# Kernel tuning notes

Measured on AMD Instinct MI355X. Metric: run time of the kernel, lower is better.

Reference implementation:

```python
import jax, jax.numpy as jnp
import numpy as np


def conv2d(x, w, b, pad):
    # NCHW conv, stride 1, symmetric padding
    out = jax.lax.conv_general_dilated(
        x, w, window_strides=(1, 1), padding=[(pad, pad), (pad, pad)],
        dimension_numbers=("NCHW", "OIHW", "NCHW"))
    return out + b[None, :, None, None]


def setup_inputs() -> dict:
    key = jax.random.key(0)
    ks = jax.random.split(key, 18)
    B, C, H, W = 4, 256, 64, 64
    Cq = C // 16  # 16
    Ck = C // 8   # 32
    s = 0.02
    return {
        "x": jax.random.normal(ks[0], (B, C, H, W), jnp.float32),
        "dw1_w": jax.random.normal(ks[1], (Cq, C, 7, 7), jnp.float32) * s,
        "dw1_b": jnp.zeros((Cq,), jnp.float32),
        "dw2_w": jax.random.normal(ks[2], (Cq, C, 11, 11), jnp.float32) * s,
        "dw2_b": jnp.zeros((Cq,), jnp.float32),
        "key_w": jax.random.normal(ks[3], (Ck, C, 1, 1), jnp.float32) * s,
        "key_b": jnp.zeros((Ck,), jnp.float32),
        "value_w": jax.random.normal(ks[4], (C, C, 1, 1), jnp.float32) * s,
        "value_b": jnp.zeros((C,), jnp.float32),
        "conv1_w": jax.random.normal(ks[5], (Cq, C, 3, 3), jnp.float32) * s,
        "conv1_b": jnp.zeros((Cq,), jnp.float32),
        "conv2_w": jax.random.normal(ks[6], (C, Cq, 3, 3), jnp.float32) * s,
        "conv2_b": jnp.zeros((C,), jnp.float32),
        "se_w": jax.random.normal(ks[7], (C, C, 1, 1), jnp.float32) * s,
        "se_b": jnp.zeros((C,), jnp.float32),
        "gamma1": jnp.zeros((1,), jnp.float32) + 0.1,  # nonzero so attention path is exercised
        "gamma2": jnp.zeros((1,), jnp.float32) + 0.1,
    }


def reference(x, dw1_w, dw1_b, dw2_w, dw2_b, key_w, key_b, value_w, value_b,
              conv1_w, conv1_b, conv2_w, conv2_b, se_w, se_b, gamma1, gamma2):
    B, C, H, W = x.shape
    HW = H * W
    # q: concat of 7x7 and 11x11 conv branches -> (B, HW, C//8)
    q = jnp.concatenate([conv2d(x, dw1_w, dw1_b, 3), conv2d(x, dw2_w, dw2_b, 5)], axis=1)
    q = q.reshape(B, -1, HW).transpose(0, 2, 1)
    # k: 1x1 conv -> (B, C//8, HW)
    k = conv2d(x, key_w, key_b, 0).reshape(B, -1, HW)
    # raw (unscaled) full spatial attention, softmax over last dim
    att = jax.nn.softmax(jnp.einsum("bnc,bcm->bnm", q, k), axis=-1)  # (B, HW, HW)
    v = conv2d(x, value_w, value_b, 0).reshape(B, C, HW)
    out = jnp.einsum("bcm,bnm->bcn", v, att).reshape(B, C, H, W)
    # local conv branch + channel attention (SE)
    y = conv2d(jax.nn.silu(conv2d(x, conv1_w, conv1_b, 1)), conv2_w, conv2_b, 1)
    pooled = jnp.mean(y, axis=(2, 3), keepdims=True)  # (B, C, 1, 1)
    se = y * jax.nn.sigmoid(conv2d(pooled, se_w, se_b, 0))
    return gamma1 * out + gamma2 * se + x
```

## Files before the change

kernel.cpp:

```cpp
#include <hip/hip_runtime.h>

typedef unsigned short u16;
typedef unsigned u32;
typedef __bf16 bf16x8 __attribute__((ext_vector_type(8)));
typedef float f32x4 __attribute__((ext_vector_type(4)));
typedef float f32x16 __attribute__((ext_vector_type(16)));

#define MFMA16(A,B,C) __builtin_amdgcn_mfma_f32_16x16x32_bf16((A),(B),(C),0,0,0)
#define MFMA32(A,B,C) __builtin_amdgcn_mfma_f32_32x32x16_bf16((A),(B),(C),0,0,0)

__device__ __forceinline__ u16 f2b(float f){
  union { float f; unsigned u; } X; X.f = f;
  unsigned r = X.u + 0x7FFFu + ((X.u >> 16) & 1u);
  return (u16)(r >> 16);
}
__device__ __forceinline__ float b2f(u16 h){
  union { unsigned u; float f; } X; X.u = ((unsigned)h) << 16; return X.f;
}
__device__ __forceinline__ u16 f2b_trunc(float f){
  union { float f; unsigned u; } X; X.f = f;
  return (u16)(X.u >> 16);
}
__device__ __forceinline__ bf16x8 ld_frag(const u16* p){
  union { uint4 u; bf16x8 v; } U; U.u = *(const uint4*)p; return U.v;
}
__device__ __forceinline__ u32 pkbf(float a, float b){
  u32 r; asm("v_cvt_pk_bf16_f32 %0, %1, %2" : "=v"(r) : "v"(a), "v"(b)); return r;
}
__device__ __forceinline__ void pl32swap(u32& x, u32& y){
  auto r = __builtin_amdgcn_permlane32_swap(x, y, false, false);
  x = r[0]; y = r[1];
}
__device__ __forceinline__ void gld16(const u16* g, u16* l){
  __builtin_amdgcn_global_load_lds(
      (const __attribute__((address_space(1))) u32*)g,
      (__attribute__((address_space(3))) u32*)l, 16, 0, 0);
}

__global__ __launch_bounds__(256) void k_prep_w(
    const float* __restrict__ dw1, const float* __restrict__ dw2,
    const float* __restrict__ cw1, const float* __restrict__ kw,
    const float* __restrict__ vw,  const float* __restrict__ cw2,
    u16* __restrict__ wB, u16* __restrict__ wC,
    u16* __restrict__ kwt, u16* __restrict__ vwt, u16* __restrict__ w2t){
  int i = blockIdx.x * 256 + threadIdx.x;
  const int NB = 991232, NC = 73728, NK = 8192, NV = 65536, N2 = 40960;
  if(i < NB){
    int tap = i >> 13, rem = i & 8191;
    int chunk = rem >> 9, r2 = rem & 511;
    int oc = r2 >> 4, ci = chunk*16 + (r2 & 15);
    int dy = tap / 11, dx = tap - dy*11;
    float v;
    if(oc < 16){
      v = (dy >= 2 && dy <= 8 && dx >= 2 && dx <= 8) ? dw1[(oc*256 + ci)*49 + (dy-2)*7 + (dx-2)] : 0.f;
    } else {
      v = dw2[((oc-16)*256 + ci)*121 + tap];
    }
    wB[i] = f2b(v);
    return;
  }
  i -= NB;
  if(i < NC){
    int tap = i >> 13, rem = i & 8191;
    int chunk = rem >> 9, r2 = rem & 511;
    int oc = r2 >> 4, ci = chunk*16 + (r2 & 15);
    wC[i] = (oc < 16) ? f2b(cw1[(oc*256 + ci)*9 + tap]) : (u16)0;
    return;
  }
  i -= NC;
  if(i < NK){ kwt[i] = f2b(kw[i]); return; }
  i -= NK;
  if(i < NV){ vwt[i] = f2b(vw[i]); return; }
  i -= NV;
  if(i < N2){
    int co = i/160, kk = i - co*160;
    int tap = kk >> 4, ci = kk & 15;
    w2t[i] = (tap < 9) ? f2b(cw2[co*144 + ci*9 + tap]) : (u16)0;
    return;
  }
}

__global__ __launch_bounds__(256) void k_prep_x(const float* __restrict__ x, u16* __restrict__ xp){
  __shared__ float tile[32][33];
  const int bid = blockIdx.x;
  const int b = bid >> 10, rem = bid & 1023;
  const int c0 = (rem >> 7) << 5, m0 = (rem & 127) << 5;
  const int t = threadIdx.x;
  { const int cg = t >> 5, mm = t & 31;
    #pragma unroll
    for(int i=0;i<4;i++)
      tile[cg*4+i][mm] = x[((size_t)(b*256 + c0 + cg*4 + i) << 12) + m0 + mm];
  }
  __syncthreads();
  { const int cp = (t & 15) << 1, mloc = t >> 4;
    #pragma unroll
    for(int half = 0; half < 2; ++half){
      const int ml = half*16 + mloc;
      const int m = m0 + ml;
      const int yy = (m >> 6) + 5, xx = (m & 63) + 5;
      const int ci = c0 + cp;
      const int chunk = ci >> 4, wi = ci & 15;
      u16 lo = f2b(tile[cp][ml]), hi = f2b(tile[cp+1][ml]);
      *(unsigned*)&xp[(((size_t)(b*16 + chunk)*74 + yy)*80 + xx)*16 + wi] = ((unsigned)hi << 16) | lo;
    }
  }
}

__global__ __launch_bounds__(256) void k_qconv(
    const u16* __restrict__ xp, const u16* __restrict__ wB, const u16* __restrict__ wC,
    u16* __restrict__ qp){
  __shared__ __align__(16) u16 buf[15360];
  const int bid = blockIdx.x;
  const int rg = bid & 31, b = (bid >> 5) & 3, kq = bid >> 7;
  const int y0 = rg << 1;
  const int t = threadIdx.x, wv = t >> 6, lane = t & 63;
  const int m = lane & 31, kh = lane >> 5;
  const int laneoff = m*16 + kh*8;
  const int r = wv & 1, xo = (wv >> 1) << 5;
  const f32x16 z16 = {0.f,0.f,0.f,0.f,0.f,0.f,0.f,0.f,0.f,0.f,0.f,0.f,0.f,0.f,0.f,0.f};
  f32x16 acc = z16, acc1 = z16;

  #pragma unroll 1
  for(int c = 0; c < 2; ++c){
    const int chunk = kq*2 + c;
    const uint4* src = (const uint4*)(xp + ((size_t)((b*16 + chunk)*74 + y0))*1280);
    __syncthreads();
    for(int e = t; e < 1920; e += 256){
      ((uint4*)buf)[(e & 1)*960 + (e >> 1)] = src[e];
    }
    __syncthreads();
    const u16* wBc = wB + chunk*512 + laneoff;
    const u16* wCc = wC + chunk*512 + laneoff;
    const u16* ap = buf + kh*7680 + (r*80 + xo + m)*8;
    #pragma unroll 1
    for(int dy = 0; dy < 11; ++dy){
      const u16* rowp = ap + dy*640;
      const u16* wrow = wBc + dy*11*8192;
      const bool in1y = (dy >= 4) & (dy <= 6);
      #pragma unroll
      for(int dx = 0; dx < 11; ++dx){
        bf16x8 A = ld_frag(rowp + dx*8);
        bf16x8 B = ld_frag(wrow + dx*8192);
        acc = MFMA32(A, B, acc);
        if(in1y && dx >= 4 && dx <= 6){
          bf16x8 B1 = ld_frag(wCc + ((dy-4)*3 + (dx-4))*8192);
          acc1 = MFMA32(A, B1, acc1);
        }
      }
    }
  }

  u16* qb = qp + ((size_t)kq*16384 + (b << 12) + (y0 + r)*64 + xo) * 48;
  #pragma unroll
  for(int reg = 0; reg < 16; ++reg){
    const int row = (reg & 3) + ((reg >> 2) << 3) + (kh << 2);
    qb[row*48 + m] = f2b(acc[reg]);
    if(m < 16) qb[row*48 + 32 + m] = f2b(acc1[reg]);
  }
}

__global__ __launch_bounds__(256) void k_qfin(
    const u16* __restrict__ qp, const float* __restrict__ b7,
    const float* __restrict__ b11, const float* __restrict__ b1,
    u16* __restrict__ q_t, u16* __restrict__ t1){
  const int t = threadIdx.x, wv = t >> 6, lane = t & 63;
  const int px = blockIdx.x*4 + wv;
  if(lane >= 48) return;
  const size_t off = (size_t)px*48 + lane;
  float s = 0.f;
  #pragma unroll
  for(int sp = 0; sp < 8; ++sp) s += b2f(qp[off + (size_t)sp*786432]);
  const float LOG2E = 1.44269504f;
  if(lane < 16){
    q_t[px*32 + lane] = f2b((s + b7[lane]) * LOG2E);
  } else if(lane < 32){
    q_t[px*32 + lane] = f2b((s + b11[lane - 16]) * LOG2E);
  } else {
    float v = s + b1[lane - 32];
    t1[px*16 + lane - 32] = f2b(v / (1.f + __expf(-v)));
  }
}

__global__ __launch_bounds__(256) void k_kv(
    const u16* __restrict__ xp, const u16* __restrict__ vwt, const u16* __restrict__ kwt,
    const float* __restrict__ vb, const float* __restrict__ kb,
    u16* __restrict__ vt, u16* __restrict__ k_t){
  const int bid = blockIdx.x;
  const int h = bid & 3, blk = (bid >> 2) & 63, b = bid >> 8;
  const int wv = threadIdx.x >> 6, lane = threadIdx.x & 63;
  const int col = lane & 15, quad = lane >> 4;
  const int m0 = (blk << 6) + (wv << 4);
  f32x4 z = {0.f,0.f,0.f,0.f};
  f32x4 av[4], ak[2];
  #pragma unroll
  for(int i=0;i<4;i++) av[i] = z;
  ak[0] = z; ak[1] = z;
  const int m = m0 + col;
  const int py = (m >> 6) + 5, pxx = (m & 63) + 5;
  #pragma unroll 1
  for(int ch = 0; ch < 8; ++ch){
    const int cio = ch*32 + quad*8;
    const int chunk = cio >> 4, wi = cio & 15;
    bf16x8 xf = ld_frag(xp + (((size_t)(b*16 + chunk)*74 + py)*80 + pxx)*16 + wi);
    #pragma unroll
    for(int ct2 = 0; ct2 < 4; ++ct2){
      bf16x8 wf = ld_frag(vwt + (((h*4 + ct2)*16 + col) << 8) + cio);
      av[ct2] = MFMA16(wf, xf, av[ct2]);
    }
    if(h == 0){
      #pragma unroll
      for(int kt = 0; kt < 2; ++kt){
        bf16x8 kf = ld_frag(kwt + ((kt*16 + col) << 8) + cio);
        ak[kt] = MFMA16(xf, kf, ak[kt]);
      }
    }
  }
  const int g = m0 >> 5, lo = (m0 & 31) + col;
  #pragma unroll
  for(int ct2 = 0; ct2 < 4; ++ct2){
    #pragma unroll
    for(int r = 0; r < 4; ++r){
      const int c = (h*4 + ct2)*16 + quad*4 + r;
      vt[((size_t)(b*128 + g)*256 + c)*32 + lo] = f2b(av[ct2][r] + vb[c]);
    }
  }
  if(h == 0){
    #pragma unroll
    for(int kt = 0; kt < 2; ++kt){
      #pragma unroll
      for(int r = 0; r < 4; ++r){
        const int mq = b*4096 + m0 + quad*4 + r;
        k_t[mq*32 + kt*16 + col] = f2b((ak[kt][r] + kb[kt*16 + col]) );
      }
    }
  }
}

__global__ __launch_bounds__(512, 4) void k_attn(
    const u16* __restrict__ q_t, const u16* __restrict__ k_t,
    const u16* __restrict__ vt, u16* __restrict__ Op,
    float* __restrict__ lsav){
  __shared__ __align__(16) u16 V[2][16384];
  const int bid = blockIdx.x;
  const int q0 = (bid & 31) << 7, b = (bid >> 5) & 3, ks = bid >> 7;
  const int t = threadIdx.x, wv = t >> 6, lane = t & 63;
  const int cq = lane & 31, hi = lane >> 5;
  const int wq = wv >> 1, ch = wv & 1;
  const int swz = (cq & 7) << 4;
  const int cbase = (ch*128 + cq) * 128;

  const u16* qrow = q_t + ((size_t)(b*4096 + q0 + wq*32 + cq) << 5) + hi*8;
  const bf16x8 qf0 = ld_frag(qrow), qf1 = ld_frag(qrow + 16);
  const u16* kbase = k_t + ((size_t)(b*4096 + ks*1024 + cq) << 5) + hi*8;
  const u16* vsrc = vt + ((size_t)(b*128 + ks*32) << 13);

  u32 srcoff[4];
  #pragma unroll
  for(int s = 0; s < 4; ++s){
    const int idx = s*512 + t;
    const int c = idx >> 3;
    const int rs = ((idx & 7) << 4) ^ ((c & 7) << 4);
    srcoff[s] = ((rs >> 6) << 13) + (c << 5) + ((rs & 63) >> 1);
  }

  const f32x16 z16 = {0.f,0.f,0.f,0.f,0.f,0.f,0.f,0.f,0.f,0.f,0.f,0.f,0.f,0.f,0.f,0.f};
  f32x16 acc0 = z16, acc1 = z16, acc2 = z16, acc3 = z16;
  float lsum = 0.f;

  #pragma unroll
  for(int s = 0; s < 4; ++s)
    gld16(vsrc + srcoff[s], &V[0][s*4096 + (wv << 9)]);
  __syncthreads();

  #pragma unroll 1
  for(int it = 0; it < 16; ++it){
    const int cur = it & 1;
    if(it < 15){
      const u16* gb = vsrc + ((size_t)(it + 1) << 14);
      #pragma unroll
      for(int s = 0; s < 4; ++s)
        gld16(gb + srcoff[s], &V[cur ^ 1][s*4096 + (wv << 9)]);
    }
    const u16* kp = kbase + ((size_t)it << 11);
    const u16* Vb = &V[cur][0];
    #pragma unroll
    for(int sub = 0; sub < 2; ++sub){
      const bf16x8 kf0 = ld_frag(kp + sub*1024);
      const bf16x8 kf1 = ld_frag(kp + sub*1024 + 16);
      f32x16 S = MFMA32(kf0, qf0, z16);
      S = MFMA32(kf1, qf1, S);
      #pragma unroll
      for(int rr = 0; rr < 16; ++rr){ S[rr] = exp2f(S[rr]); lsum += S[rr]; }
      u32 a0 = pkbf(S[0], S[1]),   b0 = pkbf(S[4], S[5]);
      u32 a1 = pkbf(S[2], S[3]),   b1 = pkbf(S[6], S[7]);
      u32 c0 = pkbf(S[8], S[9]),   d0 = pkbf(S[12], S[13]);
      u32 c1 = pkbf(S[10], S[11]), d1 = pkbf(S[14], S[15]);
      pl32swap(a0, b0); pl32swap(a1, b1); pl32swap(c0, d0); pl32swap(c1, d1);
      union { u32 w[4]; bf16x8 v; } A0, A1;
      A0.w[0] = a0; A0.w[1] = a1; A0.w[2] = b0; A0.w[3] = b1;
      A1.w[0] = c0; A1.w[1] = c1; A1.w[2] = d0; A1.w[3] = d1;
      const int o0 = cbase + ((((sub << 6) | (hi << 4))) ^ swz);
      const char* vb0 = (const char*)Vb + o0;
      const char* vb1 = (const char*)Vb + (o0 ^ 32);
      acc0 = MFMA32(A0.v, ld_frag((const u16*)(vb0)),         acc0);
      acc1 = MFMA32(A0.v, ld_frag((const u16*)(vb0 + 4096)),  acc1);
      acc2 = MFMA32(A0.v, ld_frag((const u16*)(vb0 + 8192)),  acc2);
      acc3 = MFMA32(A0.v, ld_frag((const u16*)(vb0 + 12288)), acc3);
      acc0 = MFMA32(A1.v, ld_frag((const u16*)(vb1)),         acc0);
      acc1 = MFMA32(A1.v, ld_frag((const u16*)(vb1 + 4096)),  acc1);
      acc2 = MFMA32(A1.v, ld_frag((const u16*)(vb1 + 8192)),  acc2);
      acc3 = MFMA32(A1.v, ld_frag((const u16*)(vb1 + 12288)), acc3);
    }
    __syncthreads();
  }

  lsum += __shfl_xor(lsum, 32);
  const float invl = 1.f / lsum;
  if(ch == 0 && hi == 0)
    lsav[ks*16384 + b*4096 + q0 + wq*32 + cq] = lsum;
  u16* ob = Op + (((size_t)(ks*16384 + b*4096 + q0 + wq*32)) << 8) + ch*128 + cq;
  #pragma unroll
  for(int reg = 0; reg < 16; ++reg){
    const int row = (reg & 3) + ((reg >> 2) << 3) + (hi << 2);
    const float inv = __shfl(invl, row);
    u16* orow = ob + ((size_t)row << 8);
    orow[0]  = f2b(acc0[reg] * inv);
    orow[32] = f2b(acc1[reg] * inv);
    orow[64] = f2b(acc2[reg] * inv);
    orow[96] = f2b(acc3[reg] * inv);
  }
}

__global__ __launch_bounds__(256) void k_conv2(
    const u16* __restrict__ t1, const u16* __restrict__ w2t, const float* __restrict__ b2,
    u16* __restrict__ y_t, float* __restrict__ pooled){
  __shared__ __align__(16) u16 im[64][168];
  __shared__ float pool_l[64];
  const int bid = blockIdx.x;
  const int h = bid & 3, y = (bid >> 2) & 63, b = bid >> 8;
  const int t = threadIdx.x;
  if(t < 64) pool_l[t] = 0.f;
  const u16* t1b = t1 + ((size_t)(b*4096) << 4);
  { const int px = t >> 2, ci0 = (t & 3) << 2;
    #pragma unroll
    for(int tap = 0; tap < 9; ++tap){
      const int ky = (tap*11) >> 5, kx = tap - ky*3;
      const int ryy = y + ky - 1, rxx = px + kx - 1;
      uint2 val = make_uint2(0u, 0u);
      if((unsigned)ryy < 64u && (unsigned)rxx < 64u)
        val = *(const uint2*)(t1b + (((ryy << 6) + rxx) << 4) + ci0);
      *(uint2*)&im[px][tap*16 + ci0] = val;
    }
    for(int e = t; e < 1024; e += 256){ im[e >> 4][144 + (e & 15)] = 0; }
  }
  __syncthreads();
  const int wv = t >> 6, lane = t & 63, col = lane & 15, quad = lane >> 4;
  const f32x4 z = {0.f,0.f,0.f,0.f};
  f32x4 acc[4];
  #pragma unroll
  for(int i=0;i<4;i++) acc[i] = z;
  #pragma unroll
  for(int ch = 0; ch < 5; ++ch){
    bf16x8 af = ld_frag(&im[wv*16 + col][ch*32 + quad*8]);
    #pragma unroll
    for(int j = 0; j < 4; ++j){
      bf16x8 wf = ld_frag(w2t + ((h*4 + j)*16 + col)*160 + ch*32 + quad*8);
      acc[j] = MFMA16(af, wf, acc[j]);
    }
  }
  const int m0 = (y << 6) + (wv << 4) + (quad << 2);
  #pragma unroll
  for(int j = 0; j < 4; ++j){
    const int c = (h*4 + j)*16 + col;
    const float bias = b2[c];
    float s = 0.f;
    #pragma unroll
    for(int r = 0; r < 4; ++r){
      float v = acc[j][r] + bias;
      y_t[((size_t)(b*4096 + m0 + r) << 8) + c] = f2b(v);
      s += v;
    }
    s += __shfl_xor(s, 16); s += __shfl_xor(s, 32);
    if(quad == 0) atomicAdd(&pool_l[c - h*64], s);
  }
  __syncthreads();
  if(t < 64) atomicAdd(&pooled[b*256 + h*64 + t], pool_l[t]);
}

__global__ __launch_bounds__(256) void k_final(
    const u16* __restrict__ Op, const u16* __restrict__ y_t, const float* __restrict__ x,
    const float* __restrict__ lsav, const float* __restrict__ pooled,
    const float* __restrict__ sew, const float* __restrict__ seb,
    const float* __restrict__ g1p, const float* __restrict__ g2p,
    float* __restrict__ out){
  __shared__ float tO[32][65];
  __shared__ float tY[32][65];
  __shared__ float gate_l[32];
  const int bid = blockIdx.x;
  const int b = bid >> 9, rem = bid & 511;
  const int c0 = (rem >> 6) << 5, m0 = (rem & 63) << 6;
  const int t = threadIdx.x;
  const float g1 = g1p[0], g2 = g2p[0];
  { const int cl = t >> 3, k0 = (t & 7) << 5;
    const int c = c0 + cl;
    const float* wr = sew + (size_t)c*256 + k0;
    const float* pr = pooled + b*256 + k0;
    float part = 0.f;
    #pragma unroll
    for(int j = 0; j < 32; j += 4){
      float4 w4 = *(const float4*)(wr + j);
      float4 p4 = *(const float4*)(pr + j);
      part += w4.x*p4.x + w4.y*p4.y + w4.z*p4.z + w4.w*p4.w;
    }
    part += __shfl_xor(part, 1); part += __shfl_xor(part, 2); part += __shfl_xor(part, 4);
    if((t & 7) == 0){
      float a = part * (1.f/4096.f) + seb[c];
      gate_l[cl] = g2 / (1.f + __expf(-a));
    }
  }
  { const int ml = t >> 2, cg = (t & 3) << 3;
    const int gq = b*4096 + m0 + ml;
    const float l0 = lsav[gq], l1 = lsav[16384 + gq], l2 = lsav[32768 + gq], l3 = lsav[49152 + gq];
    const float inv = 1.f / (l0 + l1 + l2 + l3);
    const float w0 = l0*inv, w1 = l1*inv, w2 = l2*inv, w3 = l3*inv;
    const size_t base = ((size_t)gq << 8) + c0 + cg;
    union { uint4 u; u16 s[8]; } A0, A1, A2, A3;
    A0.u = *(const uint4*)(Op + base);
    A1.u = *(const uint4*)(Op + base + ((size_t)16384 << 8));
    A2.u = *(const uint4*)(Op + base + ((size_t)32768 << 8));
    A3.u = *(const uint4*)(Op + base + ((size_t)49152 << 8));
    #pragma unroll
    for(int i = 0; i < 8; ++i)
      tO[cg+i][ml] = w0*b2f(A0.s[i]) + w1*b2f(A1.s[i]) + w2*b2f(A2.s[i]) + w3*b2f(A3.s[i]);
    const u16* yrow = y_t + base;
    uint4 yu = *(const uint4*)yrow;
    tY[cg+0][ml]=b2f((u16)(yu.x & 0xffffu)); tY[cg+1][ml]=b2f((u16)(yu.x >> 16));
    tY[cg+2][ml]=b2f((u16)(yu.y & 0xffffu)); tY[cg+3][ml]=b2f((u16)(yu.y >> 16));
    tY[cg+4][ml]=b2f((u16)(yu.z & 0xffffu)); tY[cg+5][ml]=b2f((u16)(yu.z >> 16));
    tY[cg+6][ml]=b2f((u16)(yu.w & 0xffffu)); tY[cg+7][ml]=b2f((u16)(yu.w >> 16));
  }
  __syncthreads();
  { const int cl = t >> 3, mg = (t & 7) << 3;
    const int c = c0 + cl;
    const float gate = gate_l[cl];
    const float* xrow = x + ((size_t)(b*256 + c) << 12) + m0 + mg;
    float* orow = out + ((size_t)(b*256 + c) << 12) + m0 + mg;
    float4 x0 = *(const float4*)xrow, x1 = *(const float4*)(xrow + 4);
    float4 r0, r1;
    r0.x = g1*tO[cl][mg+0] + gate*tY[cl][mg+0] + x0.x;
    r0.y = g1*tO[cl][mg+1] + gate*tY[cl][mg+1] + x0.y;
    r0.z = g1*tO[cl][mg+2] + gate*tY[cl][mg+2] + x0.z;
    r0.w = g1*tO[cl][mg+3] + gate*tY[cl][mg+3] + x0.w;
    r1.x = g1*tO[cl][mg+4] + gate*tY[cl][mg+4] + x1.x;
    r1.y = g1*tO[cl][mg+5] + gate*tY[cl][mg+5] + x1.y;
    r1.z = g1*tO[cl][mg+6] + gate*tY[cl][mg+6] + x1.z;
    r1.w = g1*tO[cl][mg+7] + gate*tY[cl][mg+7] + x1.w;
    *(float4*)orow = r0;
    *(float4*)(orow + 4) = r1;
  }
}

extern "C" void kernel_launch(void* const* d_in, const int* in_sizes, int n_in,
                              void* d_out, int out_size, void* d_ws, size_t ws_size,
                              hipStream_t stream){
  (void)in_sizes; (void)n_in; (void)out_size; (void)ws_size;
  const float* x    = (const float*)d_in[0];
  const float* dw1w = (const float*)d_in[1];
  const float* dw1b = (const float*)d_in[2];
  const float* dw2w = (const float*)d_in[3];
  const float* dw2b = (const float*)d_in[4];
  const float* keyw = (const float*)d_in[5];
  const float* keyb = (const float*)d_in[6];
  const float* valw = (const float*)d_in[7];
  const float* valb = (const float*)d_in[8];
  const float* c1w  = (const float*)d_in[9];
  const float* c1b  = (const float*)d_in[10];
  const float* c2w  = (const float*)d_in[11];
  const float* c2b  = (const float*)d_in[12];
  const float* sew  = (const float*)d_in[13];
  const float* seb  = (const float*)d_in[14];
  const float* g1   = (const float*)d_in[15];
  const float* g2   = (const float*)d_in[16];
  float* out = (float*)d_out;

  char* w = (char*)d_ws;
  auto take = [&](size_t bytes) -> char* {
    char* p = w; w += (bytes + 255) & ~(size_t)255; return p;
  };
  u16*  Op   = (u16*)  take(33554432);
  u16*  q_t  = (u16*)  take(1048576);
  u16*  k_t  = (u16*)  take(1048576);
  u16*  vt   = (u16*)  take(8388608);
  u16*  t1   = (u16*)  take(524288);
  u16*  y_t  = (u16*)  take(8388608);
  u16*  kwt  = (u16*)  take(16384);
  u16*  vwt  = (u16*)  take(131072);
  u16*  w2t  = (u16*)  take(81920);
  float* pooled = (float*)take(4096);
  float* lsav   = (float*)take(262144);

  u16*  xp = Op;
  u16*  qp = Op + 6062080;
  u16*  wB = vt;
  u16*  wC = vt + 991232;

  hipMemsetAsync(xp, 0, 12124160, stream);
  hipMemsetAsync(pooled, 0, 4096, stream);
  k_prep_w<<<4608, 256, 0, stream>>>(dw1w, dw2w, c1w, keyw, valw, c2w, wB, wC, kwt, vwt, w2t);
  k_prep_x<<<4096, 256, 0, stream>>>(x, xp);
  k_qconv<<<1024, 256, 0, stream>>>(xp, wB, wC, qp);
  k_qfin<<<4096, 256, 0, stream>>>(qp, dw1b, dw2b, c1b, q_t, t1);
  k_kv<<<1024, 256, 0, stream>>>(xp, vwt, kwt, valb, keyb, vt, k_t);
  k_attn<<<512, 512, 0, stream>>>(q_t, k_t, vt, Op, lsav);
  k_conv2<<<1024, 256, 0, stream>>>(t1, w2t, c2b, y_t, pooled);
  k_final<<<2048, 256, 0, stream>>>(Op, y_t, x, lsav, pooled, sew, seb, g1, g2, out);
}
```

Measured before the change: 292.1 us.

## Re-layout V into MFMA fragment order and give each attention wave all 256 channels

The k_kv kernel now writes V directly in the per-lane fragment order that the attention MFMA B-operand reads, so the LDS tile can be filled with plain linear global-to-LDS copies and read without XOR swizzling. k_attn drops from 8 to 4 waves per block. Each wave now computes its 32 query rows against all 256 output channels with 8 accumulators, so the QK^T and exp work is no longer duplicated across two channel-half waves. The row-sum is split into four partial accumulators to shorten the dependency chain. The cost is higher register pressure (128 accumulator floats per lane) and possible LDS bank conflicts from the unswizzled layout.

```diff
diff --git a/kernel.cpp b/kernel.cpp
--- a/kernel.cpp
+++ b/kernel.cpp
@@ -16,10 +16,6 @@
 }
 __device__ __forceinline__ float b2f(u16 h){
   union { unsigned u; float f; } X; X.u = ((unsigned)h) << 16; return X.f;
-}
-__device__ __forceinline__ u16 f2b_trunc(float f){
-  union { float f; unsigned u; } X; X.f = f;
-  return (u16)(X.u >> 16);
 }
 __device__ __forceinline__ bf16x8 ld_frag(const u16* p){
   union { uint4 u; bf16x8 v; } U; U.u = *(const uint4*)p; return U.v;
@@ -215,13 +211,14 @@
       }
     }
   }
-  const int g = m0 >> 5, lo = (m0 & 31) + col;
+  const size_t kgb = ((size_t)(b*256 + (m0 >> 4)));
+  const int hi2 = col >> 3, j = col & 7;
   #pragma unroll
   for(int ct2 = 0; ct2 < 4; ++ct2){
     #pragma unroll
     for(int r = 0; r < 4; ++r){
       const int c = (h*4 + ct2)*16 + quad*4 + r;
-      vt[((size_t)(b*128 + g)*256 + c)*32 + lo] = f2b(av[ct2][r] + vb[c]);
+      vt[((((kgb*8 + (c >> 5))*2 + hi2)*32) + (c & 31))*8 + j] = f2b(av[ct2][r] + vb[c]);
     }
   }
   if(h == 0){
@@ -236,7 +233,7 @@
   }
 }
 
-__global__ __launch_bounds__(512, 4) void k_attn(
+__global__ __launch_bounds__(256, 2) void k_attn(
     const u16* __restrict__ q_t, const u16* __restrict__ k_t,
     const u16* __restrict__ vt, u16* __restrict__ Op,
     float* __restrict__ lsav){
@@ -245,31 +242,21 @@
   const int q0 = (bid & 31) << 7, b = (bid >> 5) & 3, ks = bid >> 7;
   const int t = threadIdx.x, wv = t >> 6, lane = t & 63;
   const int cq = lane & 31, hi = lane >> 5;
-  const int wq = wv >> 1, ch = wv & 1;
-  const int swz = (cq & 7) << 4;
-  const int cbase = (ch*128 + cq) * 128;
-
-  const u16* qrow = q_t + ((size_t)(b*4096 + q0 + wq*32 + cq) << 5) + hi*8;
+
+  const u16* qrow = q_t + ((size_t)(b*4096 + q0 + wv*32 + cq) << 5) + hi*8;
   const bf16x8 qf0 = ld_frag(qrow), qf1 = ld_frag(qrow + 16);
   const u16* kbase = k_t + ((size_t)(b*4096 + ks*1024 + cq) << 5) + hi*8;
-  const u16* vsrc = vt + ((size_t)(b*128 + ks*32) << 13);
-
-  u32 srcoff[4];
-  #pragma unroll
-  for(int s = 0; s < 4; ++s){
-    const int idx = s*512 + t;
-    const int c = idx >> 3;
-    const int rs = ((idx & 7) << 4) ^ ((c & 7) << 4);
-    srcoff[s] = ((rs >> 6) << 13) + (c << 5) + ((rs & 63) >> 1);
-  }
+  const u16* vsrc = vt + ((size_t)(b*256 + ks*64) << 12);
 
   const f32x16 z16 = {0.f,0.f,0.f,0.f,0.f,0.f,0.f,0.f,0.f,0.f,0.f,0.f,0.f,0.f,0.f,0.f};
-  f32x16 acc0 = z16, acc1 = z16, acc2 = z16, acc3 = z16;
-  float lsum = 0.f;
-
-  #pragma unroll
-  for(int s = 0; s < 4; ++s)
-    gld16(vsrc + srcoff[s], &V[0][s*4096 + (wv << 9)]);
+  f32x16 acc[8];
+  #pragma unroll
+  for(int i=0;i<8;i++) acc[i] = z16;
+  float lp0=0.f, lp1=0.f, lp2=0.f, lp3=0.f;
+
+  #pragma unroll
+  for(int s = 0; s < 8; ++s)
+    gld16(vsrc + (size_t)(s*256 + t)*8, &V[0][(s*256 + (wv << 6))*8]);
   __syncthreads();
 
   #pragma unroll 1
@@ -278,56 +265,56 @@
     if(it < 15){
       const u16* gb = vsrc + ((size_t)(it + 1) << 14);
       #pragma unroll
-      for(int s = 0; s < 4; ++s)
-        gld16(gb + srcoff[s], &V[cur ^ 1][s*4096 + (wv << 9)]);
+      for(int s = 0; s < 8; ++s)
+        gld16(gb + (size_t)(s*256 + t)*8, &V[cur ^ 1][(s*256 + (wv << 6))*8]);
     }
     const u16* kp = kbase + ((size_t)it << 11);
-    const u16* Vb = &V[cur][0];
+    const u16* Vb = &V[cur][hi*256 + cq*8];
     #pragma unroll
     for(int sub = 0; sub < 2; ++sub){
       const bf16x8 kf0 = ld_frag(kp + sub*1024);
       const bf16x8 kf1 = ld_frag(kp + sub*1024 + 16);
       f32x16 S = MFMA32(kf0, qf0, z16);
       S = MFMA32(kf1, qf1, S);
-      #pragma unroll
-      for(int rr = 0; rr < 16; ++rr){ S[rr] = exp2f(S[rr]); lsum += S[rr]; }
-      u32 a0 = pkbf(S[0], S[1]),   b0 = pkbf(S[4], S[5]);
-      u32 a1 = pkbf(S[2], S[3]),   b1 = pkbf(S[6], S[7]);
-      u32 c0 = pkbf(S[8], S[9]),   d0 = pkbf(S[12], S[13]);
-      u32 c1 = pkbf(S[10], S[11]), d1 = pkbf(S[14], S[15]);
+      float p[16];
+      #pragma unroll
+      for(int rr = 0; rr < 16; ++rr) p[rr] = exp2f(S[rr]);
+      #pragma unroll
+      for(int rr = 0; rr < 16; rr += 4){
+        lp0 += p[rr]; lp1 += p[rr+1]; lp2 += p[rr+2]; lp3 += p[rr+3];
+      }
+      u32 a0 = pkbf(p[0], p[1]),   b0 = pkbf(p[4], p[5]);
+      u32 a1 = pkbf(p[2], p[3]),   b1 = pkbf(p[6], p[7]);
+      u32 c0 = pkbf(p[8], p[9]),   d0 = pkbf(p[12], p[13]);
+      u32 c1 = pkbf(p[10], p[11]), d1 = pkbf(p[14], p[15]);
       pl32swap(a0, b0); pl32swap(a1, b1); pl32swap(c0, d0); pl32swap(c1, d1);
       union { u32 w[4]; bf16x8 v; } A0, A1;
       A0.w[0] = a0; A0.w[1] = a1; A0.w[2] = b0; A0.w[3] = b1;
       A1.w[0] = c0; A1.w[1] = c1; A1.w[2] = d0; A1.w[3] = d1;
-      const int o0 = cbase + ((((sub << 6) | (hi << 4))) ^ swz);
-      const char* vb0 = (const char*)Vb + o0;
-      const char* vb1 = (const char*)Vb + (o0 ^ 32);
-      acc0 = MFMA32(A0.v, ld_frag((const u16*)(vb0)),         acc0);
-      acc1 = MFMA32(A0.v, ld_frag((const u16*)(vb0 + 4096)),  acc1);
-      acc2 = MFMA32(A0.v, ld_frag((const u16*)(vb0 + 8192)),  acc2);
-      acc3 = MFMA32(A0.v, ld_frag((const u16*)(vb0 + 12288)), acc3);
-      acc0 = MFMA32(A1.v, ld_frag((const u16*)(vb1)),         acc0);
-      acc1 = MFMA32(A1.v, ld_frag((const u16*)(vb1 + 4096)),  acc1);
-      acc2 = MFMA32(A1.v, ld_frag((const u16*)(vb1 + 8192)),  acc2);
-      acc3 = MFMA32(A1.v, ld_frag((const u16*)(vb1 + 12288)), acc3);
+      const u16* f0 = Vb + sub*8192;
+      #pragma unroll
+      for(int ct = 0; ct < 8; ++ct){
+        acc[ct] = MFMA32(A0.v, ld_frag(f0 + ct*512),        acc[ct]);
+        acc[ct] = MFMA32(A1.v, ld_frag(f0 + 4096 + ct*512), acc[ct]);
+      }
     }
     __syncthreads();
   }
 
-  lsum += __shfl_xor(lsum, 32);
-  const float invl = 1.f / lsum;
-  if(ch == 0 && hi == 0)
-    lsav[ks*16384 + b*4096 + q0 + wq*32 + cq] = lsum;
-  u16* ob = Op + (((size_t)(ks*16384 + b*4096 + q0 + wq*32)) << 8) + ch*128 + cq;
+  float lt = lp0 + lp1 + lp2 + lp3;
+  lt += __shfl_xor(lt, 32);
+  if(lane < 32)
+    lsav[ks*16384 + b*4096 + q0 + wv*32 + cq] = lt;
+  const float invl = 1.f / lt;
+  u16* ob = Op + (((size_t)(ks*16384 + b*4096 + q0 + wv*32)) << 8) + cq;
   #pragma unroll
   for(int reg = 0; reg < 16; ++reg){
     const int row = (reg & 3) + ((reg >> 2) << 3) + (hi << 2);
     const float inv = __shfl(invl, row);
     u16* orow = ob + ((size_t)row << 8);
-    orow[0]  = f2b(acc0[reg] * inv);
-    orow[32] = f2b(acc1[reg] * inv);
-    orow[64] = f2b(acc2[reg] * inv);
-    orow[96] = f2b(acc3[reg] * inv);
+    #pragma unroll
+    for(int ct = 0; ct < 8; ++ct)
+      orow[ct*32] = f2b(acc[ct][reg] * inv);
   }
 }
 
@@ -511,7 +498,7 @@
   k_qconv<<<1024, 256, 0, stream>>>(xp, wB, wC, qp);
   k_qfin<<<4096, 256, 0, stream>>>(qp, dw1b, dw2b, c1b, q_t, t1);
   k_kv<<<1024, 256, 0, stream>>>(xp, vwt, kwt, valb, keyb, vt, k_t);
-  k_attn<<<512, 512, 0, stream>>>(q_t, k_t, vt, Op, lsav);
+  k_attn<<<512, 256, 0, stream>>>(q_t, k_t, vt, Op, lsav);
   k_conv2<<<1024, 256, 0, stream>>>(t1, w2t, c2b, y_t, pooled);
   k_final<<<2048, 256, 0, stream>>>(Op, y_t, x, lsav, pooled, sew, seb, g1, g2, out);
 }
```

Result: faster. 280.7 us (-3.9%).
